# Optimization experiments

Hardware: AMD Instinct MI355X
Metric: run time of the kernel (lower is better)

Reference implementation:

```python
import jax, jax.numpy as jnp
import numpy as np

N = 50000      # total nodes in batch
E = 640000     # directed edges
G = 64         # graphs in batch
F_IN = 24      # node features
H = 128        # hidden dim
L = 4          # num GCN layers
BN_EPS = 1e-5


def setup_inputs() -> dict:
    key = jax.random.key(0)
    ks = jax.random.split(key, 12)
    s = 0.05  # weight init scale
    return {
        "x": jax.random.normal(ks[0], (N, F_IN), jnp.float32),
        "edge_index": jax.random.randint(ks[1], (2, E), 0, N, dtype=jnp.int32),
        "batch": jnp.sort(jax.random.randint(ks[2], (N,), 0, G, dtype=jnp.int32)),
        "W0": jax.random.normal(ks[3], (F_IN, H), jnp.float32) * s,
        "Wh": jax.random.normal(ks[4], (L - 1, H, H), jnp.float32) * s,
        "b": jnp.zeros((L, H), jnp.float32),
        "bn_gamma": jnp.ones((L, H), jnp.float32),
        "bn_beta": jnp.zeros((L, H), jnp.float32),
        "bn_mean": jax.random.normal(ks[5], (L, H), jnp.float32) * 0.01,
        "bn_var": jnp.ones((L, H), jnp.float32),
        "pool_W": jax.random.normal(ks[6], (2 * H, H), jnp.float32) * s,
        "pool_b": jnp.zeros((H,), jnp.float32),
        "out_W": jax.random.normal(ks[7], (H, H // 2), jnp.float32) * s,
        "out_b": jnp.zeros((H // 2,), jnp.float32),
    }


def reference(x, edge_index, batch, W0, Wh, b, bn_gamma, bn_beta, bn_mean,
              bn_var, pool_W, pool_b, out_W, out_b):
    n = x.shape[0]
    loop = jnp.arange(n, dtype=edge_index.dtype)
    src = jnp.concatenate([edge_index[0], loop])  # [E+N] with self-loops
    dst = jnp.concatenate([edge_index[1], loop])
    # symmetric GCN normalization: deg includes self-loops, so deg >= 1
    deg = jax.ops.segment_sum(jnp.ones_like(dst, x.dtype), dst, num_segments=n)
    dis = jax.lax.rsqrt(deg)
    coef = (dis[src] * dis[dst])[:, None]  # [E+N, 1]

    def gcn_conv(h, W, bias):
        h = h @ W                                   # [N, H]
        msg = h[src] * coef                         # gather + scale
        return jax.ops.segment_sum(msg, dst, num_segments=n) + bias

    Ws = [W0] + [Wh[i] for i in range(Wh.shape[0])]
    h = x
    for i in range(L):
        h = gcn_conv(h, Ws[i], b[i])
        # BatchNorm1d (eval mode) + ReLU; dropout = identity in eval
        h = (h - bn_mean[i]) * jax.lax.rsqrt(bn_var[i] + BN_EPS) * bn_gamma[i] + bn_beta[i]
        h = jax.nn.relu(h)

    counts = jax.ops.segment_sum(jnp.ones((n,), h.dtype), batch, num_segments=G)
    x_mean = jax.ops.segment_sum(h, batch, num_segments=G) / jnp.maximum(counts, 1.0)[:, None]
    x_max = jax.ops.segment_max(h, batch, num_segments=G)
    x_pooled = jnp.concatenate([x_mean, x_max], axis=1)        # [G, 2H]
    x_pooled = jax.nn.relu(x_pooled @ pool_W + pool_b)         # global_pool MLP
    return x_pooled @ out_W + out_b                            # embedding head [G, H//2]
```

## Files before the change

kernel.cpp:

```cpp
#include <hip/hip_runtime.h>
#include <hip/hip_bf16.h>
#include <hip/hip_fp16.h>

#define HD 128
#define BN_EPS 1e-5f

typedef __attribute__((ext_vector_type(8))) short short8;
typedef __attribute__((ext_vector_type(8))) _Float16 half8;
typedef __attribute__((ext_vector_type(4))) float f32x4;

__device__ inline unsigned short f2bf(float v, float& rem) {
    unsigned u = __float_as_uint(v);
    unsigned r = (u + 0x7FFFu + ((u >> 16) & 1u)) >> 16;
    rem = v - __uint_as_float(r << 16);
    return (unsigned short)r;
}

__global__ void k_count(const int* __restrict__ dst, int* __restrict__ counts,
                        unsigned short* __restrict__ ord, int E) {
    int i = blockIdx.x * blockDim.x + threadIdx.x;
    for (; i < E; i += gridDim.x * blockDim.x) {
        int pos = atomicAdd(&counts[dst[i]], 1);
        ord[i] = (unsigned short)pos;
    }
}

__global__ void k_scan1(const int* __restrict__ counts, int* __restrict__ offs,
                        int* __restrict__ bsums, int n) {
    __shared__ int s[256];
    int t = threadIdx.x, i = blockIdx.x * 256 + t;
    int v = (i < n) ? counts[i] : 0;
    s[t] = v; __syncthreads();
    for (int d = 1; d < 256; d <<= 1) {
        int x = (t >= d) ? s[t - d] : 0;
        __syncthreads(); s[t] += x; __syncthreads();
    }
    if (i < n) offs[i] = s[t] - v;
    if (t == 255) bsums[blockIdx.x] = s[255];
}

__global__ void k_scan2(int* __restrict__ bsums, int nb,
                        const int* __restrict__ batch, int* __restrict__ starts,
                        int n, int G) {
    __shared__ int s[256];
    int t = threadIdx.x;
    int v = (t < nb) ? bsums[t] : 0;
    s[t] = v; __syncthreads();
    for (int d = 1; d < 256; d <<= 1) {
        int x = (t >= d) ? s[t - d] : 0;
        __syncthreads(); s[t] += x; __syncthreads();
    }
    if (t < nb) bsums[t] = s[t] - v;
    if (t <= G) {
        int lo = 0, hi = n;
        while (lo < hi) {
            int mid = (lo + hi) >> 1;
            if (batch[mid] < t) lo = mid + 1; else hi = mid;
        }
        starts[t] = lo;
    }
}

__global__ void k_scan3(int* __restrict__ offs, const int* __restrict__ bsums,
                        const int* __restrict__ counts, float* __restrict__ dis, int n) {
    int i = blockIdx.x * 256 + threadIdx.x;
    if (i < n) {
        offs[i] += bsums[blockIdx.x];
        dis[i] = rsqrtf((float)(counts[i] + 1));
    }
}

__global__ void k_fill(const int* __restrict__ src, const int* __restrict__ dst,
                       const unsigned short* __restrict__ ord, const int* __restrict__ offs,
                       unsigned short* __restrict__ esrc, int E) {
    int i = blockIdx.x * blockDim.x + threadIdx.x;
    for (; i < E; i += gridDim.x * blockDim.x) {
        int s = src[i], d = dst[i];
        esrc[offs[d] + ord[i]] = (unsigned short)s;
    }
}

__global__ void k_wsplit(const float* __restrict__ W0, const float* __restrict__ Wh,
                         unsigned short* __restrict__ whi0, unsigned short* __restrict__ wlo0,
                         unsigned short* __restrict__ whf, unsigned short* __restrict__ wlf) {
    int idx = blockIdx.x * 256 + threadIdx.x;
    int l = idx >> 14, rest = idx & 16383;
    int k = rest >> 7, c = rest & 127;
    int cb = c >> 4, kc = k >> 5;
    int lane = (c & 15) | (((k & 31) >> 3) << 4);
    int j = k & 7;
    if (l == 0) {
        if (k >= 32) return;
        float val = (k < 24) ? W0[k * HD + c] : 0.f;
        float rem, rem2;
        unsigned short hi = f2bf(val, rem);
        unsigned short lo = f2bf(rem, rem2);
        size_t addr = (size_t)(cb * 64 + lane) * 8 + j;
        whi0[addr] = hi; wlo0[addr] = lo;
    } else {
        float val = Wh[(size_t)(l - 1) * HD * HD + (size_t)k * HD + c];
        __half h = __float2half(val);
        float rem = val - __half2float(h);
        __half lo = __float2half(rem);
        size_t addr = (size_t)(l - 1) * 16384 + (size_t)((cb * 4 + kc) * 64 + lane) * 8 + j;
        whf[addr] = __half_as_ushort(h);
        wlf[addr] = __half_as_ushort(lo);
    }
}

__global__ void k_agg_x(const float* __restrict__ in, const int* __restrict__ offs,
                        const int* __restrict__ counts, const unsigned short* __restrict__ esrc,
                        const float* __restrict__ dis, unsigned short* __restrict__ ohi,
                        unsigned short* __restrict__ olo, int n) {
    const int FQ = 6, GRP = 8;
    int grp = threadIdx.x / GRP;
    int lane = threadIdx.x % GRP;
    int node = blockIdx.x * (blockDim.x / GRP) + grp;
    if (node >= n) return;
    int rowblk = node >> 4, rr = node & 15;

    if (lane == FQ) {
        size_t base = (size_t)rowblk * 512 + (size_t)(rr + 48) * 8;
        ushort4 z = make_ushort4(0, 0, 0, 0);
        *(ushort4*)(ohi + base) = z; *(ushort4*)(ohi + base + 4) = z;
        *(ushort4*)(olo + base) = z; *(ushort4*)(olo + base + 4) = z;
    }
    if (lane >= FQ) return;

    const float4* in4 = reinterpret_cast<const float4*>(in);
    float dn = dis[node];
    float sl = dn * dn;
    float4 a = in4[(size_t)node * FQ + lane];
    float4 accA = make_float4(sl * a.x, sl * a.y, sl * a.z, sl * a.w);
    float4 accB = make_float4(0.f, 0.f, 0.f, 0.f);

    int e = offs[node], end = e + counts[node];
    for (; e + 3 < end; e += 4) {
        int s0 = esrc[e],     s1 = esrc[e + 1];
        int s2 = esrc[e + 2], s3 = esrc[e + 3];
        float c0 = dis[s0] * dn, c1 = dis[s1] * dn;
        float c2 = dis[s2] * dn, c3 = dis[s3] * dn;
        float4 v0 = in4[(size_t)s0 * FQ + lane];
        float4 v1 = in4[(size_t)s1 * FQ + lane];
        float4 v2 = in4[(size_t)s2 * FQ + lane];
        float4 v3 = in4[(size_t)s3 * FQ + lane];
        accA.x = fmaf(c0, v0.x, fmaf(c2, v2.x, accA.x));
        accA.y = fmaf(c0, v0.y, fmaf(c2, v2.y, accA.y));
        accA.z = fmaf(c0, v0.z, fmaf(c2, v2.z, accA.z));
        accA.w = fmaf(c0, v0.w, fmaf(c2, v2.w, accA.w));
        accB.x = fmaf(c1, v1.x, fmaf(c3, v3.x, accB.x));
        accB.y = fmaf(c1, v1.y, fmaf(c3, v3.y, accB.y));
        accB.z = fmaf(c1, v1.z, fmaf(c3, v3.z, accB.z));
        accB.w = fmaf(c1, v1.w, fmaf(c3, v3.w, accB.w));
    }
    for (; e < end; ++e) {
        int s0 = esrc[e];
        float c0 = dis[s0] * dn;
        float4 v0 = in4[(size_t)s0 * FQ + lane];
        accA.x = fmaf(c0, v0.x, accA.x);
        accA.y = fmaf(c0, v0.y, accA.y);
        accA.z = fmaf(c0, v0.z, accA.z);
        accA.w = fmaf(c0, v0.w, accA.w);
    }
    float4 acc = make_float4(accA.x + accB.x, accA.y + accB.y,
                             accA.z + accB.z, accA.w + accB.w);

    int f0 = lane * 4;
    int lidx = rr | (((f0 & 31) >> 3) << 4);
    int j0 = f0 & 7;
    size_t base = (size_t)rowblk * 512 + (size_t)lidx * 8 + j0;
    float r0, r1, r2, r3, d0;
    ushort4 hi, lo;
    hi.x = f2bf(acc.x, r0); hi.y = f2bf(acc.y, r1);
    hi.z = f2bf(acc.z, r2); hi.w = f2bf(acc.w, r3);
    lo.x = f2bf(r0, d0); lo.y = f2bf(r1, d0);
    lo.z = f2bf(r2, d0); lo.w = f2bf(r3, d0);
    *(ushort4*)(ohi + base) = hi;
    *(ushort4*)(olo + base) = lo;
}

__global__ void k_agg_h(const __half* __restrict__ in, const int* __restrict__ offs,
                        const int* __restrict__ counts, const unsigned short* __restrict__ esrc,
                        const float* __restrict__ dis, unsigned short* __restrict__ af, int n) {
    int grp = threadIdx.x >> 5;
    int lane = threadIdx.x & 31;
    int node = blockIdx.x * 8 + grp;
    if (node >= n) return;
    int rowblk = node >> 4, rr = node & 15;

    const float2* in8 = reinterpret_cast<const float2*>(in);
    float dn = dis[node];
    float sl = dn * dn;

    float2 raw = in8[(size_t)node * 32 + lane];
    __half2 p0 = *(__half2*)&raw.x, p1 = *(__half2*)&raw.y;
    float2 f0v = __half22float2(p0), f1v = __half22float2(p1);
    float4 accA = make_float4(sl * f0v.x, sl * f0v.y, sl * f1v.x, sl * f1v.y);
    float4 accB = make_float4(0.f, 0.f, 0.f, 0.f);

    int e = offs[node], end = e + counts[node];
    for (; e + 3 < end; e += 4) {
        int s0 = esrc[e],     s1 = esrc[e + 1];
        int s2 = esrc[e + 2], s3 = esrc[e + 3];
        float c0 = dis[s0] * dn, c1 = dis[s1] * dn;
        float c2 = dis[s2] * dn, c3 = dis[s3] * dn;
        float2 w0 = in8[(size_t)s0 * 32 + lane];
        float2 w1 = in8[(size_t)s1 * 32 + lane];
        float2 w2 = in8[(size_t)s2 * 32 + lane];
        float2 w3 = in8[(size_t)s3 * 32 + lane];
        float2 a0 = __half22float2(*(__half2*)&w0.x), b0 = __half22float2(*(__half2*)&w0.y);
        float2 a1 = __half22float2(*(__half2*)&w1.x), b1 = __half22float2(*(__half2*)&w1.y);
        float2 a2 = __half22float2(*(__half2*)&w2.x), b2 = __half22float2(*(__half2*)&w2.y);
        float2 a3 = __half22float2(*(__half2*)&w3.x), b3 = __half22float2(*(__half2*)&w3.y);
        accA.x = fmaf(c0, a0.x, fmaf(c2, a2.x, accA.x));
        accA.y = fmaf(c0, a0.y, fmaf(c2, a2.y, accA.y));
        accA.z = fmaf(c0, b0.x, fmaf(c2, b2.x, accA.z));
        accA.w = fmaf(c0, b0.y, fmaf(c2, b2.y, accA.w));
        accB.x = fmaf(c1, a1.x, fmaf(c3, a3.x, accB.x));
        accB.y = fmaf(c1, a1.y, fmaf(c3, a3.y, accB.y));
        accB.z = fmaf(c1, b1.x, fmaf(c3, b3.x, accB.z));
        accB.w = fmaf(c1, b1.y, fmaf(c3, b3.y, accB.w));
    }
    for (; e < end; ++e) {
        int s0 = esrc[e];
        float c0 = dis[s0] * dn;
        float2 w0 = in8[(size_t)s0 * 32 + lane];
        float2 a0 = __half22float2(*(__half2*)&w0.x), b0 = __half22float2(*(__half2*)&w0.y);
        accA.x = fmaf(c0, a0.x, accA.x);
        accA.y = fmaf(c0, a0.y, accA.y);
        accA.z = fmaf(c0, b0.x, accA.z);
        accA.w = fmaf(c0, b0.y, accA.w);
    }
    float4 acc = make_float4(accA.x + accB.x, accA.y + accB.y,
                             accA.z + accB.z, accA.w + accB.w);

    int f0 = lane * 4;
    int kc = f0 >> 5;
    int lidx = rr | (((f0 & 31) >> 3) << 4);
    int j0 = f0 & 7;
    size_t base = ((size_t)rowblk * 4 + kc) * 512 + (size_t)lidx * 8 + j0;
    ushort4 hv;
    hv.x = __half_as_ushort(__float2half(acc.x));
    hv.y = __half_as_ushort(__float2half(acc.y));
    hv.z = __half_as_ushort(__float2half(acc.z));
    hv.w = __half_as_ushort(__float2half(acc.w));
    *(ushort4*)(af + base) = hv;
}

__global__ __launch_bounds__(256) void k_gemm_m(
        const unsigned short* __restrict__ agh, const unsigned short* __restrict__ agl,
        const unsigned short* __restrict__ wh, const unsigned short* __restrict__ wl,
        const float* __restrict__ bias, const float* __restrict__ gamma,
        const float* __restrict__ beta, const float* __restrict__ mean,
        const float* __restrict__ var, __half* __restrict__ outh, int n) {
    __shared__ unsigned short lbh[8 * 512];
    __shared__ unsigned short lbl[8 * 512];
    int tid = threadIdx.x;
    for (int i = tid; i < 1024; i += 256) {
        ((ushort4*)lbh)[i] = ((const ushort4*)wh)[i];
        ((ushort4*)lbl)[i] = ((const ushort4*)wl)[i];
    }
    __syncthreads();

    int wave = tid >> 6, lane = tid & 63;
    int grb0 = blockIdx.x * 8 + wave * 2;

    f32x4 acc[2][8] = {};

    short8 a0h = *(const short8*)(agh + (size_t)grb0 * 512 + lane * 8);
    short8 a0l = *(const short8*)(agl + (size_t)grb0 * 512 + lane * 8);
    short8 a1h = *(const short8*)(agh + (size_t)(grb0 + 1) * 512 + lane * 8);
    short8 a1l = *(const short8*)(agl + (size_t)(grb0 + 1) * 512 + lane * 8);
    #pragma unroll
    for (int cb = 0; cb < 8; ++cb) {
        short8 bh = *(const short8*)(lbh + (size_t)(cb * 64 + lane) * 8);
        short8 bl = *(const short8*)(lbl + (size_t)(cb * 64 + lane) * 8);
        acc[0][cb] = __builtin_amdgcn_mfma_f32_16x16x32_bf16(a0h, bh, acc[0][cb], 0, 0, 0);
        acc[0][cb] = __builtin_amdgcn_mfma_f32_16x16x32_bf16(a0h, bl, acc[0][cb], 0, 0, 0);
        acc[0][cb] = __builtin_amdgcn_mfma_f32_16x16x32_bf16(a0l, bh, acc[0][cb], 0, 0, 0);
        acc[1][cb] = __builtin_amdgcn_mfma_f32_16x16x32_bf16(a1h, bh, acc[1][cb], 0, 0, 0);
        acc[1][cb] = __builtin_amdgcn_mfma_f32_16x16x32_bf16(a1h, bl, acc[1][cb], 0, 0, 0);
        acc[1][cb] = __builtin_amdgcn_mfma_f32_16x16x32_bf16(a1l, bh, acc[1][cb], 0, 0, 0);
    }

    int colbase = lane & 15;
    float scv[8], shv[8];
    #pragma unroll
    for (int cb = 0; cb < 8; ++cb) {
        int c = cb * 16 + colbase;
        float s = gamma[c] * rsqrtf(var[c] + BN_EPS);
        scv[cb] = s;
        shv[cb] = beta[c] + (bias[c] - mean[c]) * s;
    }
    int r0 = (lane >> 4) * 4;
    #pragma unroll
    for (int rb = 0; rb < 2; ++rb) {
        int rowb = (grb0 + rb) * 16 + r0;
        #pragma unroll
        for (int rg = 0; rg < 4; ++rg) {
            int row = rowb + rg;
            if (row < n) {
                #pragma unroll
                for (int cb = 0; cb < 8; ++cb) {
                    float v = fmaxf(fmaf(acc[rb][cb][rg], scv[cb], shv[cb]), 0.f);
                    outh[(size_t)row * HD + cb * 16 + colbase] = __float2half(v);
                }
            }
        }
    }
}

template<bool POOL>
__global__ __launch_bounds__(256) void k_gemm_h(
        const unsigned short* __restrict__ af,
        const unsigned short* __restrict__ wh, const unsigned short* __restrict__ wl,
        const float* __restrict__ bias, const float* __restrict__ gamma,
        const float* __restrict__ beta, const float* __restrict__ mean,
        const float* __restrict__ var, __half* __restrict__ outh,
        const int* __restrict__ batch, float* __restrict__ gsum,
        unsigned int* __restrict__ gmax, int n) {
    __shared__ unsigned short lbh[16384];
    __shared__ unsigned short lbl[16384];
    int tid = threadIdx.x;
    for (int i = tid; i < 4096; i += 256) {
        ((ushort4*)lbh)[i] = ((const ushort4*)wh)[i];
        ((ushort4*)lbl)[i] = ((const ushort4*)wl)[i];
    }
    __syncthreads();

    int wave = tid >> 6, lane = tid & 63;
    int grb0 = blockIdx.x * 8 + wave * 2;

    f32x4 acc[2][8] = {};

    #pragma unroll
    for (int kc = 0; kc < 4; ++kc) {
        half8 a0 = *(const half8*)(af + ((size_t)grb0 * 4 + kc) * 512 + lane * 8);
        half8 a1 = *(const half8*)(af + ((size_t)(grb0 + 1) * 4 + kc) * 512 + lane * 8);
        #pragma unroll
        for (int cb = 0; cb < 8; ++cb) {
            half8 bh = *(const half8*)(lbh + (size_t)((cb * 4 + kc) * 64 + lane) * 8);
            half8 bl = *(const half8*)(lbl + (size_t)((cb * 4 + kc) * 64 + lane) * 8);
            acc[0][cb] = __builtin_amdgcn_mfma_f32_16x16x32_f16(a0, bh, acc[0][cb], 0, 0, 0);
            acc[0][cb] = __builtin_amdgcn_mfma_f32_16x16x32_f16(a0, bl, acc[0][cb], 0, 0, 0);
            acc[1][cb] = __builtin_amdgcn_mfma_f32_16x16x32_f16(a1, bh, acc[1][cb], 0, 0, 0);
            acc[1][cb] = __builtin_amdgcn_mfma_f32_16x16x32_f16(a1, bl, acc[1][cb], 0, 0, 0);
        }
    }

    int colbase = lane & 15;
    float scv[8], shv[8];
    #pragma unroll
    for (int cb = 0; cb < 8; ++cb) {
        int c = cb * 16 + colbase;
        float s = gamma[c] * rsqrtf(var[c] + BN_EPS);
        scv[cb] = s;
        shv[cb] = beta[c] + (bias[c] - mean[c]) * s;
    }
    int r0 = (lane >> 4) * 4;

    if (!POOL) {
        #pragma unroll
        for (int rb = 0; rb < 2; ++rb) {
            int rowb = (grb0 + rb) * 16 + r0;
            #pragma unroll
            for (int rg = 0; rg < 4; ++rg) {
                int row = rowb + rg;
                if (row < n) {
                    #pragma unroll
                    for (int cb = 0; cb < 8; ++cb) {
                        float v = fmaxf(fmaf(acc[rb][cb][rg], scv[cb], shv[cb]), 0.f);
                        outh[(size_t)row * HD + cb * 16 + colbase] = __float2half(v);
                    }
                }
            }
        }
    } else {
        int row0 = blockIdx.x * 128;
        int row_hi = min(n - 1, row0 + 127);
        int g_lo = batch[row0];
        int g_hi = batch[row_hi];

        int gval[2][4];
        #pragma unroll
        for (int rb = 0; rb < 2; ++rb) {
            int rowb = (grb0 + rb) * 16 + r0;
            #pragma unroll
            for (int rg = 0; rg < 4; ++rg) {
                int row = rowb + rg;
                gval[rb][rg] = (row < n) ? batch[row] : -1;
            }
        }

        for (int g = g_lo; g <= g_hi; ++g) {
            #pragma unroll
            for (int cb = 0; cb < 8; ++cb) {
                float s = 0.f, m = 0.f;
                #pragma unroll
                for (int rb = 0; rb < 2; ++rb) {
                    #pragma unroll
                    for (int rg = 0; rg < 4; ++rg) {
                        if (gval[rb][rg] == g) {
                            float v = fmaxf(fmaf(acc[rb][cb][rg], scv[cb], shv[cb]), 0.f);
                            s += v;
                            m = fmaxf(m, v);
                        }
                    }
                }
                s += __shfl_xor(s, 16);
                m = fmaxf(m, __shfl_xor(m, 16));
                s += __shfl_xor(s, 32);
                m = fmaxf(m, __shfl_xor(m, 32));
                if (lane < 16 && (s != 0.f || m != 0.f)) {
                    atomicAdd(&gsum[g * HD + cb * 16 + colbase], s);
                    atomicMax(&gmax[g * HD + cb * 16 + colbase], __float_as_uint(m));
                }
            }
        }
    }
}

__global__ void k_head(const float* __restrict__ gsum, const unsigned int* __restrict__ gmax,
                       const int* __restrict__ starts, const float* __restrict__ pool_W,
                       const float* __restrict__ pool_b, const float* __restrict__ out_W,
                       const float* __restrict__ out_b, float* __restrict__ out) {
    int g = blockIdx.x, t = threadIdx.x;
    __shared__ float pooled[2 * HD];
    __shared__ float hid_s[HD];
    float cntf = fmaxf((float)(starts[g + 1] - starts[g]), 1.f);
    pooled[t] = gsum[g * HD + t] / cntf;
    pooled[HD + t] = __uint_as_float(gmax[g * HD + t]);
    __syncthreads();
    float acc = pool_b[t];
    for (int k = 0; k < 2 * HD; ++k)
        acc += pooled[k] * pool_W[k * HD + t];
    hid_s[t] = fmaxf(acc, 0.f);
    __syncthreads();
    if (t < 64) {
        float a2 = out_b[t];
        for (int j = 0; j < HD; ++j)
            a2 += hid_s[j] * out_W[j * 64 + t];
        out[g * 64 + t] = a2;
    }
}

extern "C" void kernel_launch(void* const* d_in, const int* in_sizes, int n_in,
                              void* d_out, int out_size, void* d_ws, size_t ws_size,
                              hipStream_t stream) {
    const float* x        = (const float*)d_in[0];
    const int*   eidx     = (const int*)d_in[1];
    const int*   batch    = (const int*)d_in[2];
    const float* W0       = (const float*)d_in[3];
    const float* Wh       = (const float*)d_in[4];
    const float* b        = (const float*)d_in[5];
    const float* bn_gamma = (const float*)d_in[6];
    const float* bn_beta  = (const float*)d_in[7];
    const float* bn_mean  = (const float*)d_in[8];
    const float* bn_var   = (const float*)d_in[9];
    const float* pool_W   = (const float*)d_in[10];
    const float* pool_b   = (const float*)d_in[11];
    const float* out_W    = (const float*)d_in[12];
    const float* out_b    = (const float*)d_in[13];
    float* out = (float*)d_out;

    const int N = in_sizes[2];
    const int E = in_sizes[1] / 2;
    const int L = in_sizes[5] / HD;
    const int G = out_size / (HD / 2);

    const int* src = eidx;
    const int* dst = eidx + E;

    const int NBLK = (N + 127) / 128;
    const size_t NRB = (size_t)NBLK * 8;

    char* p = (char*)d_ws;
    __half* hf   = (__half*)p; p += (size_t)NBLK * 128 * HD * 2;
    unsigned short* af  = (unsigned short*)p; p += NRB * 4 * 512 * 2;
    unsigned short* agh = (unsigned short*)p; p += NRB * 512 * 2;
    unsigned short* agl = (unsigned short*)p; p += NRB * 512 * 2;
    unsigned short* whi0 = (unsigned short*)p; p += (size_t)16384 * 2;
    unsigned short* wlo0 = (unsigned short*)p; p += (size_t)16384 * 2;
    unsigned short* whf  = (unsigned short*)p; p += (size_t)3 * 16384 * 2;
    unsigned short* wlf  = (unsigned short*)p; p += (size_t)3 * 16384 * 2;
    unsigned short* esrc = (unsigned short*)p; p += (((size_t)E * 2 + 15) & ~15ull);
    unsigned short* ord  = (unsigned short*)p; p += (((size_t)E * 2 + 15) & ~15ull);
    int*   counts  = (int*)p;   p += (size_t)N * 4;
    float* dis     = (float*)p; p += (size_t)N * 4;
    int*   offs    = (int*)p;   p += (size_t)(N + 1) * 4;
    int*   bsums   = (int*)p;   p += 256 * 4;
    float* gsum    = (float*)p; p += (size_t)G * HD * 4;
    unsigned int* gmax = (unsigned int*)p; p += (size_t)G * HD * 4;
    int*   starts  = (int*)p;   p += (size_t)(G + 1) * 4;
    (void)ws_size; (void)n_in;

    hipMemsetAsync(counts, 0, (size_t)N * 4, stream);
    hipMemsetAsync(gsum, 0, (size_t)G * HD * 8, stream);

    const int NB = (N + 255) / 256;

    k_count<<<1024, 256, 0, stream>>>(dst, counts, ord, E);
    k_scan1<<<NB, 256, 0, stream>>>(counts, offs, bsums, N);
    k_scan2<<<1, 256, 0, stream>>>(bsums, NB, batch, starts, N, G);
    k_scan3<<<NB, 256, 0, stream>>>(offs, bsums, counts, dis, N);
    k_fill<<<1024, 256, 0, stream>>>(src, dst, ord, offs, esrc, E);
    k_wsplit<<<256, 256, 0, stream>>>(W0, Wh, whi0, wlo0, whf, wlf);

    k_agg_x<<<(N + 31) / 32, 256, 0, stream>>>(x, offs, counts, esrc, dis, agh, agl, N);
    k_gemm_m<<<NBLK, 256, 0, stream>>>(agh, agl, whi0, wlo0, b, bn_gamma, bn_beta,
                                       bn_mean, bn_var, hf, N);

    for (int l = 1; l < L; ++l) {
        k_agg_h<<<(N + 7) / 8, 256, 0, stream>>>(hf, offs, counts, esrc, dis, af, N);
        const unsigned short* wh_l = whf + (size_t)(l - 1) * 16384;
        const unsigned short* wl_l = wlf + (size_t)(l - 1) * 16384;
        if (l < L - 1)
            k_gemm_h<false><<<NBLK, 256, 0, stream>>>(af, wh_l, wl_l,
                b + l * HD, bn_gamma + l * HD, bn_beta + l * HD,
                bn_mean + l * HD, bn_var + l * HD, hf, batch, gsum, gmax, N);
        else
            k_gemm_h<true><<<NBLK, 256, 0, stream>>>(af, wh_l, wl_l,
                b + l * HD, bn_gamma + l * HD, bn_beta + l * HD,
                bn_mean + l * HD, bn_var + l * HD, nullptr, batch, gsum, gmax, N);
    }

    k_head<<<G, HD, 0, stream>>>(gsum, gmax, starts, pool_W, pool_b, out_W, out_b, out);
}
```

Measured before the change: 237.8 us.

## Double hidden GEMM rows per block, fuse fill and weight split kernels

The hidden-layer GEMM now processes 256 rows per block (4 row-blocks per wave) so each LDS-loaded weight tile is reused across twice as many rows, which halves the number of blocks that reload the 64 KB of split weights. The edge fill and weight split kernels are merged into one launch, and the two memsets are combined by placing gsum/gmax right after counts. This trades more accumulator registers (possibly lower occupancy) and fewer blocks for less weight staging and launch overhead. Buffers are resized to the padded 256-row grid.

```diff
diff --git a/kernel.cpp b/kernel.cpp
--- a/kernel.cpp
+++ b/kernel.cpp
@@ -70,41 +70,43 @@
     }
 }
 
-__global__ void k_fill(const int* __restrict__ src, const int* __restrict__ dst,
-                       const unsigned short* __restrict__ ord, const int* __restrict__ offs,
-                       unsigned short* __restrict__ esrc, int E) {
-    int i = blockIdx.x * blockDim.x + threadIdx.x;
-    for (; i < E; i += gridDim.x * blockDim.x) {
-        int s = src[i], d = dst[i];
-        esrc[offs[d] + ord[i]] = (unsigned short)s;
-    }
-}
-
-__global__ void k_wsplit(const float* __restrict__ W0, const float* __restrict__ Wh,
-                         unsigned short* __restrict__ whi0, unsigned short* __restrict__ wlo0,
-                         unsigned short* __restrict__ whf, unsigned short* __restrict__ wlf) {
-    int idx = blockIdx.x * 256 + threadIdx.x;
-    int l = idx >> 14, rest = idx & 16383;
-    int k = rest >> 7, c = rest & 127;
-    int cb = c >> 4, kc = k >> 5;
-    int lane = (c & 15) | (((k & 31) >> 3) << 4);
-    int j = k & 7;
-    if (l == 0) {
-        if (k >= 32) return;
-        float val = (k < 24) ? W0[k * HD + c] : 0.f;
-        float rem, rem2;
-        unsigned short hi = f2bf(val, rem);
-        unsigned short lo = f2bf(rem, rem2);
-        size_t addr = (size_t)(cb * 64 + lane) * 8 + j;
-        whi0[addr] = hi; wlo0[addr] = lo;
+#define FILL_BLOCKS 1024
+__global__ void k_fill_wsplit(const int* __restrict__ src, const int* __restrict__ dst,
+                              const unsigned short* __restrict__ ord,
+                              const int* __restrict__ offs,
+                              unsigned short* __restrict__ esrc, int E,
+                              const float* __restrict__ W0, const float* __restrict__ Wh,
+                              unsigned short* __restrict__ whi0, unsigned short* __restrict__ wlo0,
+                              unsigned short* __restrict__ whf, unsigned short* __restrict__ wlf) {
+    int bid = blockIdx.x;
+    if (bid < FILL_BLOCKS) {
+        int i = bid * 256 + threadIdx.x;
+        for (; i < E; i += FILL_BLOCKS * 256)
+            esrc[offs[dst[i]] + ord[i]] = (unsigned short)src[i];
     } else {
-        float val = Wh[(size_t)(l - 1) * HD * HD + (size_t)k * HD + c];
-        __half h = __float2half(val);
-        float rem = val - __half2float(h);
-        __half lo = __float2half(rem);
-        size_t addr = (size_t)(l - 1) * 16384 + (size_t)((cb * 4 + kc) * 64 + lane) * 8 + j;
-        whf[addr] = __half_as_ushort(h);
-        wlf[addr] = __half_as_ushort(lo);
+        int idx = (bid - FILL_BLOCKS) * 256 + threadIdx.x;
+        int l = idx >> 14, rest = idx & 16383;
+        int k = rest >> 7, c = rest & 127;
+        int cb = c >> 4, kc = k >> 5;
+        int lane = (c & 15) | (((k & 31) >> 3) << 4);
+        int j = k & 7;
+        if (l == 0) {
+            if (k >= 32) return;
+            float val = (k < 24) ? W0[k * HD + c] : 0.f;
+            float rem, rem2;
+            unsigned short hi = f2bf(val, rem);
+            unsigned short lo = f2bf(rem, rem2);
+            size_t addr = (size_t)(cb * 64 + lane) * 8 + j;
+            whi0[addr] = hi; wlo0[addr] = lo;
+        } else {
+            float val = Wh[(size_t)(l - 1) * HD * HD + (size_t)k * HD + c];
+            __half h = __float2half(val);
+            float rem = val - __half2float(h);
+            __half lo = __float2half(rem);
+            size_t addr = (size_t)(l - 1) * 16384 + (size_t)((cb * 4 + kc) * 64 + lane) * 8 + j;
+            whf[addr] = __half_as_ushort(h);
+            wlf[addr] = __half_as_ushort(lo);
+        }
     }
 }
 
@@ -329,14 +331,16 @@
     __syncthreads();
 
     int wave = tid >> 6, lane = tid & 63;
-    int grb0 = blockIdx.x * 8 + wave * 2;
-
-    f32x4 acc[2][8] = {};
+    int grb0 = blockIdx.x * 16 + wave * 4;
+
+    f32x4 acc[4][8] = {};
 
     #pragma unroll
     for (int kc = 0; kc < 4; ++kc) {
-        half8 a0 = *(const half8*)(af + ((size_t)grb0 * 4 + kc) * 512 + lane * 8);
+        half8 a0 = *(const half8*)(af + ((size_t)(grb0 + 0) * 4 + kc) * 512 + lane * 8);
         half8 a1 = *(const half8*)(af + ((size_t)(grb0 + 1) * 4 + kc) * 512 + lane * 8);
+        half8 a2 = *(const half8*)(af + ((size_t)(grb0 + 2) * 4 + kc) * 512 + lane * 8);
+        half8 a3 = *(const half8*)(af + ((size_t)(grb0 + 3) * 4 + kc) * 512 + lane * 8);
         #pragma unroll
         for (int cb = 0; cb < 8; ++cb) {
             half8 bh = *(const half8*)(lbh + (size_t)((cb * 4 + kc) * 64 + lane) * 8);
@@ -345,6 +349,10 @@
             acc[0][cb] = __builtin_amdgcn_mfma_f32_16x16x32_f16(a0, bl, acc[0][cb], 0, 0, 0);
             acc[1][cb] = __builtin_amdgcn_mfma_f32_16x16x32_f16(a1, bh, acc[1][cb], 0, 0, 0);
             acc[1][cb] = __builtin_amdgcn_mfma_f32_16x16x32_f16(a1, bl, acc[1][cb], 0, 0, 0);
+            acc[2][cb] = __builtin_amdgcn_mfma_f32_16x16x32_f16(a2, bh, acc[2][cb], 0, 0, 0);
+            acc[2][cb] = __builtin_amdgcn_mfma_f32_16x16x32_f16(a2, bl, acc[2][cb], 0, 0, 0);
+            acc[3][cb] = __builtin_amdgcn_mfma_f32_16x16x32_f16(a3, bh, acc[3][cb], 0, 0, 0);
+            acc[3][cb] = __builtin_amdgcn_mfma_f32_16x16x32_f16(a3, bl, acc[3][cb], 0, 0, 0);
         }
     }
 
@@ -361,7 +369,7 @@
 
     if (!POOL) {
         #pragma unroll
-        for (int rb = 0; rb < 2; ++rb) {
+        for (int rb = 0; rb < 4; ++rb) {
             int rowb = (grb0 + rb) * 16 + r0;
             #pragma unroll
             for (int rg = 0; rg < 4; ++rg) {
@@ -376,14 +384,14 @@
             }
         }
     } else {
-        int row0 = blockIdx.x * 128;
-        int row_hi = min(n - 1, row0 + 127);
-        int g_lo = batch[row0];
+        int row0 = blockIdx.x * 256;
+        int row_hi = min(n - 1, row0 + 255);
+        int g_lo = batch[min(row0, n - 1)];
         int g_hi = batch[row_hi];
 
-        int gval[2][4];
+        int gval[4][4];
         #pragma unroll
-        for (int rb = 0; rb < 2; ++rb) {
+        for (int rb = 0; rb < 4; ++rb) {
             int rowb = (grb0 + rb) * 16 + r0;
             #pragma unroll
             for (int rg = 0; rg < 4; ++rg) {
@@ -397,7 +405,7 @@
             for (int cb = 0; cb < 8; ++cb) {
                 float s = 0.f, m = 0.f;
                 #pragma unroll
-                for (int rb = 0; rb < 2; ++rb) {
+                for (int rb = 0; rb < 4; ++rb) {
                     #pragma unroll
                     for (int rg = 0; rg < 4; ++rg) {
                         if (gval[rb][rg] == g) {
@@ -471,12 +479,14 @@
     const int* src = eidx;
     const int* dst = eidx + E;
 
-    const int NBLK = (N + 127) / 128;
-    const size_t NRB = (size_t)NBLK * 8;
+    const int NBLK  = (N + 127) / 128;
+    const int NBLK2 = (N + 255) / 256;
+    const size_t NRB  = (size_t)NBLK * 8;
+    const size_t NRB2 = (size_t)NBLK2 * 16;
 
     char* p = (char*)d_ws;
-    __half* hf   = (__half*)p; p += (size_t)NBLK * 128 * HD * 2;
-    unsigned short* af  = (unsigned short*)p; p += NRB * 4 * 512 * 2;
+    __half* hf   = (__half*)p; p += NRB2 * 16 * HD * 2;
+    unsigned short* af  = (unsigned short*)p; p += NRB2 * 4 * 512 * 2;
     unsigned short* agh = (unsigned short*)p; p += NRB * 512 * 2;
     unsigned short* agl = (unsigned short*)p; p += NRB * 512 * 2;
     unsigned short* whi0 = (unsigned short*)p; p += (size_t)16384 * 2;
@@ -486,16 +496,15 @@
     unsigned short* esrc = (unsigned short*)p; p += (((size_t)E * 2 + 15) & ~15ull);
     unsigned short* ord  = (unsigned short*)p; p += (((size_t)E * 2 + 15) & ~15ull);
     int*   counts  = (int*)p;   p += (size_t)N * 4;
+    float* gsum    = (float*)p; p += (size_t)G * HD * 4;
+    unsigned int* gmax = (unsigned int*)p; p += (size_t)G * HD * 4;
     float* dis     = (float*)p; p += (size_t)N * 4;
     int*   offs    = (int*)p;   p += (size_t)(N + 1) * 4;
     int*   bsums   = (int*)p;   p += 256 * 4;
-    float* gsum    = (float*)p; p += (size_t)G * HD * 4;
-    unsigned int* gmax = (unsigned int*)p; p += (size_t)G * HD * 4;
     int*   starts  = (int*)p;   p += (size_t)(G + 1) * 4;
     (void)ws_size; (void)n_in;
 
-    hipMemsetAsync(counts, 0, (size_t)N * 4, stream);
-    hipMemsetAsync(gsum, 0, (size_t)G * HD * 8, stream);
+    hipMemsetAsync(counts, 0, (size_t)N * 4 + (size_t)G * HD * 8, stream);
 
     const int NB = (N + 255) / 256;
 
@@ -503,8 +512,8 @@
     k_scan1<<<NB, 256, 0, stream>>>(counts, offs, bsums, N);
     k_scan2<<<1, 256, 0, stream>>>(bsums, NB, batch, starts, N, G);
     k_scan3<<<NB, 256, 0, stream>>>(offs, bsums, counts, dis, N);
-    k_fill<<<1024, 256, 0, stream>>>(src, dst, ord, offs, esrc, E);
-    k_wsplit<<<256, 256, 0, stream>>>(W0, Wh, whi0, wlo0, whf, wlf);
+    k_fill_wsplit<<<FILL_BLOCKS + 256, 256, 0, stream>>>(src, dst, ord, offs, esrc, E,
+                                                         W0, Wh, whi0, wlo0, whf, wlf);
 
     k_agg_x<<<(N + 31) / 32, 256, 0, stream>>>(x, offs, counts, esrc, dis, agh, agl, N);
     k_gemm_m<<<NBLK, 256, 0, stream>>>(agh, agl, whi0, wlo0, b, bn_gamma, bn_beta,
@@ -515,11 +524,11 @@
         const unsigned short* wh_l = whf + (size_t)(l - 1) * 16384;
         const unsigned short* wl_l = wlf + (size_t)(l - 1) * 16384;
         if (l < L - 1)
-            k_gemm_h<false><<<NBLK, 256, 0, stream>>>(af, wh_l, wl_l,
+            k_gemm_h<false><<<NBLK2, 256, 0, stream>>>(af, wh_l, wl_l,
                 b + l * HD, bn_gamma + l * HD, bn_beta + l * HD,
                 bn_mean + l * HD, bn_var + l * HD, hf, batch, gsum, gmax, N);
         else
-            k_gemm_h<true><<<NBLK, 256, 0, stream>>>(af, wh_l, wl_l,
+            k_gemm_h<true><<<NBLK2, 256, 0, stream>>>(af, wh_l, wl_l,
                 b + l * HD, bn_gamma + l * HD, bn_beta + l * HD,
                 bn_mean + l * HD, bn_var + l * HD, nullptr, batch, gsum, gmax, N);
     }
```

Result: faster. 232.6 us (-2.2%).
